# Optimization experiments

Hardware: AMD Instinct MI355X
Metric: run time of the kernel (lower is better)

## Reference

```python
import jax, jax.numpy as jnp
import numpy as np

STRIDE = 1
MAX_STRIDE = 250  # 25 * 10 default


def setup_inputs() -> dict:
    key = jax.random.key(0)
    k1, k2 = jax.random.split(key)
    T = 1_000_000
    prediction = jax.random.normal(k1, (T,), dtype=jnp.float32)
    ground_truth = jax.random.normal(k2, (T,), dtype=jnp.float32)
    return {"prediction": prediction, "ground_truth": ground_truth}


def reference(prediction, ground_truth):
    T = prediction.shape[0]
    lags = jnp.arange(0, MAX_STRIDE, STRIDE)
    idx = jnp.arange(T)

    # ground-truth statistics are lag-independent
    mean_gt = jnp.mean(ground_truth)
    var_gt = jnp.var(ground_truth, ddof=1)  # torch.var is unbiased
    v_gt = ground_truth - mean_gt

    def ccc_at_lag(n):
        # shifted pred: n leading zeros followed by prediction[:-n]
        src = idx - n
        pred = jnp.where(src >= 0, prediction[jnp.clip(src, 0)], 0.0)
        mean_pred = jnp.mean(pred)
        var_pred = jnp.var(pred, ddof=1)
        cov = jnp.mean((pred - mean_pred) * v_gt)  # population covariance
        denom = var_gt + var_pred + (mean_gt - mean_pred) ** 2
        return 2.0 * cov / denom

    cccs = jax.vmap(ccc_at_lag)(lags)  # [n_lags]
    return 1.0 - jnp.mean(cccs)
```

## Files before the change

kernel.cpp:

```cpp
#include <hip/hip_runtime.h>
#include <hip/hip_bf16.h>


#define TC 4096
#define NTHR 512
#define NLAG 256
#define NUSED 250
#define NREP 16
#define GT4 (TC / 4 + 66)
#define STATREP_OFF (NREP * NLAG)
#define COUNTER_OFF (STATREP_OFF + NREP * 16)
#define NSUB 32
#define PPAD 132

typedef float f2 __attribute__((ext_vector_type(2)));

__device__ __forceinline__ float4 ld_gt_sw(const float* s_gt, int i4) {
    int s = i4 ^ ((i4 >> 3) & 7);
    return *(const float4*)&s_gt[4 * s];
}

__device__ __forceinline__ void st_gt_sw(float* s_gt, int i4, float4 v) {
    int s = i4 ^ ((i4 >> 3) & 7);
    *(float4*)&s_gt[4 * s] = v;
}

__device__ __forceinline__ int pred_off(int i4) {
    return 4 * i4 + 4 * (i4 >> 5);
}

__device__ __forceinline__ float ld_atomic(const float* p) {
    return __hip_atomic_load(p, __ATOMIC_RELAXED, __HIP_MEMORY_SCOPE_AGENT);
}

__global__ __launch_bounds__(NTHR) void ccc_fused(const float* __restrict__ pred,
                                                  const float* __restrict__ gt,
                                                  float* __restrict__ ws,
                                                  float* __restrict__ out,
                                                  int T, int nch) {
    __shared__ __align__(16) float s_pred[NSUB * PPAD];
    __shared__ __align__(16) float s_gt[GT4 * 4];
    __shared__ __align__(16) float s_acc[NSUB][NLAG];
    __shared__ float s_red[8][4];
    __shared__ float s_stats[4];
    __shared__ float s_sp64[64];
    __shared__ unsigned s_last;

    const int tid = threadIdx.x;
    const int c = blockIdx.x;
    const int j0 = c * TC;

    float sp = 0.f, qp = 0.f, sg = 0.f, qg = 0.f;
    if (j0 + 4 * GT4 <= T) {
        #pragma unroll 2
        for (int i4 = tid; i4 < TC / 4; i4 += NTHR) {
            float4 v = *(const float4*)&pred[j0 + 4 * i4];
            *(float4*)&s_pred[pred_off(i4)] = v;
            sp += v.x + v.y + v.z + v.w;
            qp += v.x * v.x + v.y * v.y + v.z * v.z + v.w * v.w;
        }
        #pragma unroll 2
        for (int i4 = tid; i4 < GT4; i4 += NTHR) {
            float4 v = *(const float4*)&gt[j0 + 4 * i4];
            st_gt_sw(s_gt, i4, v);
            if (i4 < TC / 4) {
                sg += v.x + v.y + v.z + v.w;
                qg += v.x * v.x + v.y * v.y + v.z * v.z + v.w * v.w;
            }
        }
    } else {
        #pragma unroll 2
        for (int i4 = tid; i4 < TC / 4; i4 += NTHR) {
            int g = j0 + 4 * i4;
            float4 v = make_float4(0.f, 0.f, 0.f, 0.f);
            if (g + 3 < T) v = *(const float4*)&pred[g];
            *(float4*)&s_pred[pred_off(i4)] = v;
            sp += v.x + v.y + v.z + v.w;
            qp += v.x * v.x + v.y * v.y + v.z * v.z + v.w * v.w;
        }
        #pragma unroll 2
        for (int i4 = tid; i4 < GT4; i4 += NTHR) {
            int g = j0 + 4 * i4;
            float4 v = make_float4(0.f, 0.f, 0.f, 0.f);
            if (g + 3 < T) v = *(const float4*)&gt[g];
            st_gt_sw(s_gt, i4, v);
            if (i4 < TC / 4) {
                sg += v.x + v.y + v.z + v.w;
                qg += v.x * v.x + v.y * v.y + v.z * v.z + v.w * v.w;
            }
        }
    }
    __syncthreads();

    const int sub = tid >> 4;
    const int l = tid & 15;
    int gi = sub * 32 + 4 * l;
    const float* pbase = &s_pred[sub * PPAD];

    f2 E[10], O[9];
    {
        float4 a = ld_gt_sw(s_gt, gi);
        float4 b = ld_gt_sw(s_gt, gi + 1);
        float4 d = ld_gt_sw(s_gt, gi + 2);
        float4 e = ld_gt_sw(s_gt, gi + 3);
        float4 f = ld_gt_sw(s_gt, gi + 4);
        E[0] = f2{a.x, a.y}; E[1] = f2{a.z, a.w};
        E[2] = f2{b.x, b.y}; E[3] = f2{b.z, b.w};
        E[4] = f2{d.x, d.y}; E[5] = f2{d.z, d.w};
        E[6] = f2{e.x, e.y}; E[7] = f2{e.z, e.w};
        E[8] = f2{f.x, f.y}; E[9] = f2{f.z, f.w};
        O[0] = f2{a.y, a.z}; O[1] = f2{a.w, b.x};
        O[2] = f2{b.y, b.z}; O[3] = f2{b.w, d.x};
        O[4] = f2{d.y, d.z}; O[5] = f2{d.w, e.x};
        O[6] = f2{e.y, e.z}; O[7] = f2{e.w, f.x};
        O[8] = f2{f.y, f.z};
    }
    f2 acc2[16];
    #pragma unroll
    for (int k = 0; k < 16; ++k) acc2[k] = f2{0.f, 0.f};

    #pragma unroll 8
    for (int it = 0; it < 32; ++it) {
        float4 nw = ld_gt_sw(s_gt, gi + 5 + it);
        float4 p = *(const float4*)&pbase[4 * it];
        f2 pA = f2{p.x, p.y}, pB = f2{p.z, p.w};
        #pragma unroll
        for (int m = 0; m < 8; ++m) {
            acc2[2 * m]     = __builtin_elementwise_fma(pA, E[m],     acc2[2 * m]);
            acc2[2 * m]     = __builtin_elementwise_fma(pB, E[m + 1], acc2[2 * m]);
            acc2[2 * m + 1] = __builtin_elementwise_fma(pA, O[m],     acc2[2 * m + 1]);
            acc2[2 * m + 1] = __builtin_elementwise_fma(pB, O[m + 1], acc2[2 * m + 1]);
        }
        float w19 = E[9].y;
        #pragma unroll
        for (int q2 = 0; q2 < 8; ++q2) E[q2] = E[q2 + 2];
        E[8] = f2{nw.x, nw.y}; E[9] = f2{nw.z, nw.w};
        #pragma unroll
        for (int q2 = 0; q2 < 7; ++q2) O[q2] = O[q2 + 2];
        O[7] = f2{w19, nw.x}; O[8] = f2{nw.y, nw.z};
    }

    const int wv = tid >> 6, ln = tid & 63;
    #pragma unroll
    for (int off = 32; off > 0; off >>= 1) {
        sp += __shfl_down(sp, off, 64);
        qp += __shfl_down(qp, off, 64);
        sg += __shfl_down(sg, off, 64);
        qg += __shfl_down(qg, off, 64);
    }
    if (ln == 0) { s_red[wv][0] = sp; s_red[wv][1] = qp; s_red[wv][2] = sg; s_red[wv][3] = qg; }

    #pragma unroll
    for (int k = 0; k < 16; ++k)
        s_acc[sub][(l << 4) | (k ^ l)] = acc2[k].x + acc2[k].y;
    __syncthreads();

    const int rep = c & (NREP - 1);
    if (tid < NLAG) {
        float lagsum = 0.f;
        #pragma unroll
        for (int s2 = 0; s2 < NSUB; ++s2) lagsum += s_acc[s2][tid];
        int lag = (tid & 0xF0) | ((tid ^ (tid >> 4)) & 15);
        atomicAdd(&ws[rep * NLAG + lag], lagsum);
    }
    if (tid < 4) {
        float v = 0.f;
        #pragma unroll
        for (int w8 = 0; w8 < 8; ++w8) v += s_red[w8][tid];
        atomicAdd(&ws[STATREP_OFF + rep * 16 + tid], v);
    }

    __syncthreads();
    if (tid == 0) {
        unsigned* cnt = (unsigned*)(ws + COUNTER_OFF);
        unsigned old = __hip_atomic_fetch_add(cnt, 1u, __ATOMIC_RELAXED,
                                              __HIP_MEMORY_SCOPE_AGENT);
        unsigned want_poison = 0xAAAAAAAAu + (unsigned)(nch - 1);
        unsigned want_zero = (unsigned)(nch - 1);
        s_last = (old == want_poison || old == want_zero) ? 1u : 0u;
    }
    __syncthreads();
    if (!s_last) return;

    {
        const int lag = tid & 255, h = tid >> 8;
        float a = 0.f;
        #pragma unroll
        for (int r = 8 * h; r < 8 * h + 8; ++r) a += ld_atomic(&ws[r * NLAG + lag]);
        s_acc[h][lag] = a;
    }
    if (tid < 64) s_sp64[tid] = ld_atomic(&ws[STATREP_OFF + (tid >> 2) * 16 + (tid & 3)]);

    float tx = 0.f, tq = 0.f;
    if (tid < NLAG) {
        float t = pred[T - NLAG + tid];
        tx = t; tq = t * t;
    }
    #pragma unroll
    for (int d = 1; d < 64; d <<= 1) {
        float xs = __shfl_down(tx, d, 64);
        float qs = __shfl_down(tq, d, 64);
        if (ln + d < 64) { tx += xs; tq += qs; }
    }
    if (ln == 0) { s_red[wv][0] = tx; s_red[wv][1] = tq; }
    __syncthreads();

    if (tid < 4) {
        float s2 = 0.f;
        #pragma unroll
        for (int r = 0; r < 16; ++r) s2 += s_sp64[4 * r + tid];
        s_stats[tid] = s2;
    }
    if (tid < NLAG) {
        #pragma unroll
        for (int w2 = 1; w2 < 4; ++w2)
            if (w2 > wv) { tx += s_red[w2][0]; tq += s_red[w2][1]; }
        s_acc[2][tid] = tx;
        s_acc[3][tid] = tq;
    }
    __syncthreads();

    float v = 0.f;
    if (tid < NUSED) {
        const float Tf = (float)T;
        float sum_pred = s_stats[0], sumsq_pred = s_stats[1];
        float sum_gt = s_stats[2], sumsq_gt = s_stats[3];
        float mean_gt = sum_gt / Tf;
        float var_gt = (sumsq_gt - sum_gt * sum_gt / Tf) / (Tf - 1.f);
        float lagC = s_acc[0][tid] + s_acc[1][tid];
        float tail_s = (tid == 0) ? 0.f : s_acc[2][NLAG - tid];
        float tail_q = (tid == 0) ? 0.f : s_acc[3][NLAG - tid];
        float S = sum_pred - tail_s;
        float Q = sumsq_pred - tail_q;
        float mean_p = S / Tf;
        float var_p = (Q - S * S / Tf) / (Tf - 1.f);
        float cov = (lagC - mean_gt * S) / Tf;
        float dm = mean_gt - mean_p;
        v = 2.f * cov / (var_gt + var_p + dm * dm);
    }
    #pragma unroll
    for (int off = 32; off > 0; off >>= 1) v += __shfl_down(v, off, 64);
    if (ln == 0) s_red[wv][2] = v;
    __syncthreads();
    if (tid == 0) {
        float s2 = 0.f;
        #pragma unroll
        for (int w2 = 0; w2 < 8; ++w2) s2 += s_red[w2][2];
        out[0] = 1.f - s2 / (float)NUSED;
    }
}

extern "C" void kernel_launch(void* const* d_in, const int* in_sizes, int n_in,
                              void* d_out, int out_size, void* d_ws, size_t ws_size,
                              hipStream_t stream) {
    const float* pred = (const float*)d_in[0];
    const float* gt   = (const float*)d_in[1];
    float* out = (float*)d_out;
    float* ws  = (float*)d_ws;
    const int T = in_sizes[0];
    const int nch = (T + TC - 1) / TC;

    ccc_fused<<<nch, NTHR, 0, stream>>>(pred, gt, ws, out, T, nch);
}
```

Before: 70.00 us.

## Split tile load into two phases to overlap second-half loads with compute

The block now loads only the first half of the prediction tile and the matching ground-truth window before it starts computing. The second half is fetched into registers while the first 16-step correlation pass runs, then stored to shared memory after it. The correlation loop is factored into a helper of 16 iterations that is called twice, and the prediction layout is re-chunked to 68 floats per 16 float4s. This aims to hide global-memory latency behind arithmetic, at the cost of an extra barrier and more live registers.

```diff
diff --git a/kernel.cpp b/kernel.cpp
--- a/kernel.cpp
+++ b/kernel.cpp
@@ -8,10 +8,13 @@
 #define NUSED 250
 #define NREP 16
 #define GT4 (TC / 4 + 66)
+#define GT4_A 584
+#define PRED4 (TC / 4)
+#define PRED4_A 512
 #define STATREP_OFF (NREP * NLAG)
 #define COUNTER_OFF (STATREP_OFF + NREP * 16)
 #define NSUB 32
-#define PPAD 132
+#define CHUNK 68
 
 typedef float f2 __attribute__((ext_vector_type(2)));
 
@@ -26,77 +29,16 @@
 }
 
 __device__ __forceinline__ int pred_off(int i4) {
-    return 4 * i4 + 4 * (i4 >> 5);
+    return (i4 >> 4) * CHUNK + 4 * (i4 & 15);
 }
 
 __device__ __forceinline__ float ld_atomic(const float* p) {
     return __hip_atomic_load(p, __ATOMIC_RELAXED, __HIP_MEMORY_SCOPE_AGENT);
 }
 
-__global__ __launch_bounds__(NTHR) void ccc_fused(const float* __restrict__ pred,
-                                                  const float* __restrict__ gt,
-                                                  float* __restrict__ ws,
-                                                  float* __restrict__ out,
-                                                  int T, int nch) {
-    __shared__ __align__(16) float s_pred[NSUB * PPAD];
-    __shared__ __align__(16) float s_gt[GT4 * 4];
-    __shared__ __align__(16) float s_acc[NSUB][NLAG];
-    __shared__ float s_red[8][4];
-    __shared__ float s_stats[4];
-    __shared__ float s_sp64[64];
-    __shared__ unsigned s_last;
-
-    const int tid = threadIdx.x;
-    const int c = blockIdx.x;
-    const int j0 = c * TC;
-
-    float sp = 0.f, qp = 0.f, sg = 0.f, qg = 0.f;
-    if (j0 + 4 * GT4 <= T) {
-        #pragma unroll 2
-        for (int i4 = tid; i4 < TC / 4; i4 += NTHR) {
-            float4 v = *(const float4*)&pred[j0 + 4 * i4];
-            *(float4*)&s_pred[pred_off(i4)] = v;
-            sp += v.x + v.y + v.z + v.w;
-            qp += v.x * v.x + v.y * v.y + v.z * v.z + v.w * v.w;
-        }
-        #pragma unroll 2
-        for (int i4 = tid; i4 < GT4; i4 += NTHR) {
-            float4 v = *(const float4*)&gt[j0 + 4 * i4];
-            st_gt_sw(s_gt, i4, v);
-            if (i4 < TC / 4) {
-                sg += v.x + v.y + v.z + v.w;
-                qg += v.x * v.x + v.y * v.y + v.z * v.z + v.w * v.w;
-            }
-        }
-    } else {
-        #pragma unroll 2
-        for (int i4 = tid; i4 < TC / 4; i4 += NTHR) {
-            int g = j0 + 4 * i4;
-            float4 v = make_float4(0.f, 0.f, 0.f, 0.f);
-            if (g + 3 < T) v = *(const float4*)&pred[g];
-            *(float4*)&s_pred[pred_off(i4)] = v;
-            sp += v.x + v.y + v.z + v.w;
-            qp += v.x * v.x + v.y * v.y + v.z * v.z + v.w * v.w;
-        }
-        #pragma unroll 2
-        for (int i4 = tid; i4 < GT4; i4 += NTHR) {
-            int g = j0 + 4 * i4;
-            float4 v = make_float4(0.f, 0.f, 0.f, 0.f);
-            if (g + 3 < T) v = *(const float4*)&gt[g];
-            st_gt_sw(s_gt, i4, v);
-            if (i4 < TC / 4) {
-                sg += v.x + v.y + v.z + v.w;
-                qg += v.x * v.x + v.y * v.y + v.z * v.z + v.w * v.w;
-            }
-        }
-    }
-    __syncthreads();
-
-    const int sub = tid >> 4;
-    const int l = tid & 15;
-    int gi = sub * 32 + 4 * l;
-    const float* pbase = &s_pred[sub * PPAD];
-
+__device__ __forceinline__ void corr16(const float* __restrict__ s_gt,
+                                       const float* __restrict__ pbase,
+                                       int gi, f2* acc2) {
     f2 E[10], O[9];
     {
         float4 a = ld_gt_sw(s_gt, gi);
@@ -115,12 +57,8 @@
         O[6] = f2{e.y, e.z}; O[7] = f2{e.w, f.x};
         O[8] = f2{f.y, f.z};
     }
-    f2 acc2[16];
-    #pragma unroll
-    for (int k = 0; k < 16; ++k) acc2[k] = f2{0.f, 0.f};
-
-    #pragma unroll 8
-    for (int it = 0; it < 32; ++it) {
+    #pragma unroll
+    for (int it = 0; it < 16; ++it) {
         float4 nw = ld_gt_sw(s_gt, gi + 5 + it);
         float4 p = *(const float4*)&pbase[4 * it];
         f2 pA = f2{p.x, p.y}, pB = f2{p.z, p.w};
@@ -133,12 +71,101 @@
         }
         float w19 = E[9].y;
         #pragma unroll
-        for (int q2 = 0; q2 < 8; ++q2) E[q2] = E[q2 + 2];
+        for (int q = 0; q < 8; ++q) E[q] = E[q + 2];
         E[8] = f2{nw.x, nw.y}; E[9] = f2{nw.z, nw.w};
         #pragma unroll
-        for (int q2 = 0; q2 < 7; ++q2) O[q2] = O[q2 + 2];
+        for (int q = 0; q < 7; ++q) O[q] = O[q + 2];
         O[7] = f2{w19, nw.x}; O[8] = f2{nw.y, nw.z};
     }
+}
+
+__global__ __launch_bounds__(NTHR) void ccc_fused(const float* __restrict__ pred,
+                                                  const float* __restrict__ gt,
+                                                  float* __restrict__ ws,
+                                                  float* __restrict__ out,
+                                                  int T, int nch) {
+    __shared__ __align__(16) float s_pred[2 * NSUB * CHUNK];
+    __shared__ __align__(16) float s_gt[GT4 * 4];
+    __shared__ __align__(16) float s_acc[NSUB][NLAG];
+    __shared__ float s_red[8][4];
+    __shared__ float s_stats[4];
+    __shared__ float s_sp64[64];
+    __shared__ unsigned s_last;
+
+    const int tid = threadIdx.x;
+    const int c = blockIdx.x;
+    const int j0 = c * TC;
+    const bool interior = (j0 + 4 * GT4 <= T);
+
+    float sp = 0.f, qp = 0.f, sg = 0.f, qg = 0.f;
+    if (interior) {
+        {
+            float4 v = *(const float4*)&pred[j0 + 4 * tid];
+            *(float4*)&s_pred[pred_off(tid)] = v;
+            sp += v.x + v.y + v.z + v.w;
+            qp += v.x * v.x + v.y * v.y + v.z * v.z + v.w * v.w;
+        }
+        for (int i4 = tid; i4 < GT4_A; i4 += NTHR) {
+            float4 v = *(const float4*)&gt[j0 + 4 * i4];
+            st_gt_sw(s_gt, i4, v);
+            sg += v.x + v.y + v.z + v.w;
+            qg += v.x * v.x + v.y * v.y + v.z * v.z + v.w * v.w;
+        }
+    } else {
+        #pragma unroll 2
+        for (int i4 = tid; i4 < PRED4; i4 += NTHR) {
+            int g = j0 + 4 * i4;
+            float4 v = make_float4(0.f, 0.f, 0.f, 0.f);
+            if (g + 3 < T) v = *(const float4*)&pred[g];
+            *(float4*)&s_pred[pred_off(i4)] = v;
+            sp += v.x + v.y + v.z + v.w;
+            qp += v.x * v.x + v.y * v.y + v.z * v.z + v.w * v.w;
+        }
+        #pragma unroll 2
+        for (int i4 = tid; i4 < GT4; i4 += NTHR) {
+            int g = j0 + 4 * i4;
+            float4 v = make_float4(0.f, 0.f, 0.f, 0.f);
+            if (g + 3 < T) v = *(const float4*)&gt[g];
+            st_gt_sw(s_gt, i4, v);
+            if (i4 < PRED4) {
+                sg += v.x + v.y + v.z + v.w;
+                qg += v.x * v.x + v.y * v.y + v.z * v.z + v.w * v.w;
+            }
+        }
+    }
+    __syncthreads();
+
+    float4 pBp = make_float4(0.f, 0.f, 0.f, 0.f);
+    float4 pBg = make_float4(0.f, 0.f, 0.f, 0.f);
+    if (interior) {
+        pBp = *(const float4*)&pred[j0 + 4 * (PRED4_A + tid)];
+        if (tid < GT4 - GT4_A)
+            pBg = *(const float4*)&gt[j0 + 4 * (GT4_A + tid)];
+    }
+
+    const int sub = tid >> 4;
+    const int l = tid & 15;
+    f2 acc2[16];
+    #pragma unroll
+    for (int k = 0; k < 16; ++k) acc2[k] = f2{0.f, 0.f};
+
+    corr16(s_gt, &s_pred[sub * CHUNK], sub * 16 + 4 * l, acc2);
+
+    if (interior) {
+        *(float4*)&s_pred[pred_off(PRED4_A + tid)] = pBp;
+        sp += pBp.x + pBp.y + pBp.z + pBp.w;
+        qp += pBp.x * pBp.x + pBp.y * pBp.y + pBp.z * pBp.z + pBp.w * pBp.w;
+        if (tid < GT4 - GT4_A) {
+            st_gt_sw(s_gt, GT4_A + tid, pBg);
+            if (GT4_A + tid < PRED4) {
+                sg += pBg.x + pBg.y + pBg.z + pBg.w;
+                qg += pBg.x * pBg.x + pBg.y * pBg.y + pBg.z * pBg.z + pBg.w * pBg.w;
+            }
+        }
+    }
+    __syncthreads();
+
+    corr16(s_gt, &s_pred[(NSUB + sub) * CHUNK], 512 + sub * 16 + 4 * l, acc2);
 
     const int wv = tid >> 6, ln = tid & 63;
     #pragma unroll
```

Measured after the change: 69.52 us. Within noise of the previous version (-0.7%).
